# Kernel tuning notes

Measured on AMD Instinct MI355X. Metric: run time of the kernel, lower is better.

Reference implementation:

```python
import jax, jax.numpy as jnp
import numpy as np


def setup_inputs() -> dict:
    key = jax.random.key(0)
    ks = jax.random.split(key, 8)
    B, S, T, H, A = 4, 1024, 256, 512, 256
    return {
        "encoder_outputs": jax.random.normal(ks[0], (B, S, H), dtype=jnp.float32),
        "decoder_hidden": jax.random.normal(ks[1], (B, T, H), dtype=jnp.float32),
        "Wh": jax.random.normal(ks[2], (H, A), dtype=jnp.float32) * (1.0 / np.sqrt(H)),
        "bh": jax.random.normal(ks[3], (A,), dtype=jnp.float32) * 0.01,
        "Ws": jax.random.normal(ks[4], (H, A), dtype=jnp.float32) * (1.0 / np.sqrt(H)),
        "bs": jax.random.normal(ks[5], (A,), dtype=jnp.float32) * 0.01,
        "Wv": jax.random.normal(ks[6], (A, 1), dtype=jnp.float32) * (1.0 / np.sqrt(A)),
        "bv": jax.random.normal(ks[7], (1,), dtype=jnp.float32) * 0.01,
    }


def reference(encoder_outputs, decoder_hidden, Wh, bh, Ws, bs, Wv, bv):
    # encoder_outputs: [B, S, H], decoder_hidden: [B, T, H]
    eh = encoder_outputs @ Wh + bh          # [B, S, A]
    dh = decoder_hidden @ Ws + bs           # [B, T, A]
    # broadcast-add (torch's unsqueeze+repeat is just a broadcast), tanh, then v-projection
    energy = jnp.tanh(eh[:, None, :, :] + dh[:, :, None, :])  # [B, T, S, A]
    scores = jnp.einsum("btsa,a->bts", energy, Wv[:, 0]) + bv[0]  # [B, T, S]
    return jax.nn.softmax(scores, axis=2)
```

## Files before the change

### kernel.cpp

```cpp
#include <hip/hip_runtime.h>

#define B_ 4
#define S_ 1024
#define T_ 256
#define H_ 512
#define A_ 256

typedef __attribute__((ext_vector_type(8))) short short8;
typedef __attribute__((ext_vector_type(4))) float f32x4;

__device__ __forceinline__ float ex2(float x)   { return __builtin_amdgcn_exp2f(x); }
__device__ __forceinline__ float rcpf_(float x) { return __builtin_amdgcn_rcpf(x); }

#define K2F 2.8853900817779268f

__device__ __forceinline__ void split_bf16(float x, unsigned short& h, unsigned short& l)
{
    unsigned u = __float_as_uint(x);
    unsigned r = (u + 0x7FFFu + ((u >> 16) & 1u)) >> 16;
    h = (unsigned short)r;
    float hf = __uint_as_float(r << 16);
    float lo = x - hf;
    unsigned u2 = __float_as_uint(lo);
    l = (unsigned short)((u2 + 0x7FFFu + ((u2 >> 16) & 1u)) >> 16);
}

__global__ __launch_bounds__(256)
void prep_w(const float* __restrict__ Wh, const float* __restrict__ Wsm,
            unsigned short* __restrict__ WhTh, unsigned short* __restrict__ WhTl,
            unsigned short* __restrict__ WsTh, unsigned short* __restrict__ WsTl)
{
    __shared__ float lds[32][36];
    const int tid = threadIdx.x, bid = blockIdx.x;
    const int mat = bid >> 7, rem = bid & 127;
    const int k0 = (rem & 15) * 32, a0 = (rem >> 4) * 32;
    const float* W = mat ? Wsm : Wh;
    unsigned short* Oh = mat ? WsTh : WhTh;
    unsigned short* Ol = mat ? WsTl : WhTl;

    {
        int kl = tid >> 3, a4 = (tid & 7) * 4;
        float4 v = *(const float4*)&W[(size_t)(k0 + kl) * A_ + a0 + a4];
        lds[kl][a4] = v.x; lds[kl][a4 + 1] = v.y; lds[kl][a4 + 2] = v.z; lds[kl][a4 + 3] = v.w;
    }
    __syncthreads();
    {
        int al = tid >> 3, k4 = (tid & 7) * 4;
        unsigned short h[4], l[4];
        #pragma unroll
        for (int i = 0; i < 4; ++i) split_bf16(lds[k4 + i][al], h[i], l[i]);
        size_t o = (size_t)(a0 + al) * H_ + k0 + k4;
        *(ushort4*)&Oh[o] = make_ushort4(h[0], h[1], h[2], h[3]);
        *(ushort4*)&Ol[o] = make_ushort4(l[0], l[1], l[2], l[3]);
    }
}

__global__ __launch_bounds__(256)
void gemm_mfma(const float* __restrict__ enc, const float* __restrict__ dec,
               const unsigned short* __restrict__ WhTh, const unsigned short* __restrict__ WhTl,
               const unsigned short* __restrict__ WsTh, const unsigned short* __restrict__ WsTl,
               const float* __restrict__ bh, const float* __restrict__ bs,
               float* __restrict__ Ebuf, float* __restrict__ Dbuf)
{
    __shared__ short smem[8192];
    short* Ah = smem;
    short* Al = smem + 2048;
    short* Bh = smem + 4096;
    short* Bl = smem + 6144;

    const int tid = threadIdx.x, bid = blockIdx.x;
    const bool isE = bid < 256;
    int mb, nb;
    const float* Ag; const unsigned short* WTh; const unsigned short* WTl; const float* bias;
    if (isE) { mb = (bid & 63) * 64; nb = (bid >> 6) * 64; Ag = enc; WTh = WhTh; WTl = WhTl; bias = bh; }
    else { int b2 = bid - 256; mb = (b2 & 15) * 64; nb = (b2 >> 4) * 64; Ag = dec; WTh = WsTh; WTl = WsTl; bias = bs; }

    const int m_l = tid >> 2, q = tid & 3;
    const size_t arow = (size_t)(mb + m_l) * H_ + 8 * q;
    const size_t brow = (size_t)(nb + m_l) * H_ + 8 * q;
    const int woff = ((m_l >> 4) * 64 + (m_l & 15) + 16 * q) * 8;

    const int wave = tid >> 6, lane = tid & 63;
    const int wm = wave >> 1, wn = wave & 1;
    const int roffA = (2 * wm) * 512 + lane * 8;
    const int roffB = (2 * wn) * 512 + lane * 8;

    const int cl = lane & 15, rg = lane >> 4;
    const float bias0 = bias[nb + wn * 32 + cl];
    const float bias1 = bias[nb + wn * 32 + 16 + cl];

    f32x4 acc[2][2] = {};

    float4 aA = *(const float4*)&Ag[arow];
    float4 aB = *(const float4*)&Ag[arow + 4];
    short8 bHv = *(const short8*)&WTh[brow];
    short8 bLv = *(const short8*)&WTl[brow];

    for (int it = 0; it < 16; ++it) {
        __syncthreads();
        {
            float xs[8] = {aA.x, aA.y, aA.z, aA.w, aB.x, aB.y, aB.z, aB.w};
            short8 hv, lv;
            #pragma unroll
            for (int j = 0; j < 8; ++j) {
                unsigned short h, l; split_bf16(xs[j], h, l);
                hv[j] = (short)h; lv[j] = (short)l;
            }
            *(short8*)&Ah[woff] = hv;
            *(short8*)&Al[woff] = lv;
            *(short8*)&Bh[woff] = bHv;
            *(short8*)&Bl[woff] = bLv;
        }
        if (it < 15) {
            int kn = (it + 1) * 32;
            aA  = *(const float4*)&Ag[arow + kn];
            aB  = *(const float4*)&Ag[arow + kn + 4];
            bHv = *(const short8*)&WTh[brow + kn];
            bLv = *(const short8*)&WTl[brow + kn];
        }
        __syncthreads();
        short8 fAh0 = *(short8*)&Ah[roffA], fAh1 = *(short8*)&Ah[roffA + 512];
        short8 fAl0 = *(short8*)&Al[roffA], fAl1 = *(short8*)&Al[roffA + 512];
        short8 fBh0 = *(short8*)&Bh[roffB], fBh1 = *(short8*)&Bh[roffB + 512];
        short8 fBl0 = *(short8*)&Bl[roffB], fBl1 = *(short8*)&Bl[roffB + 512];
        acc[0][0] = __builtin_amdgcn_mfma_f32_16x16x32_bf16(fAh0, fBh0, acc[0][0], 0, 0, 0);
        acc[0][0] = __builtin_amdgcn_mfma_f32_16x16x32_bf16(fAh0, fBl0, acc[0][0], 0, 0, 0);
        acc[0][0] = __builtin_amdgcn_mfma_f32_16x16x32_bf16(fAl0, fBh0, acc[0][0], 0, 0, 0);
        acc[0][1] = __builtin_amdgcn_mfma_f32_16x16x32_bf16(fAh0, fBh1, acc[0][1], 0, 0, 0);
        acc[0][1] = __builtin_amdgcn_mfma_f32_16x16x32_bf16(fAh0, fBl1, acc[0][1], 0, 0, 0);
        acc[0][1] = __builtin_amdgcn_mfma_f32_16x16x32_bf16(fAl0, fBh1, acc[0][1], 0, 0, 0);
        acc[1][0] = __builtin_amdgcn_mfma_f32_16x16x32_bf16(fAh1, fBh0, acc[1][0], 0, 0, 0);
        acc[1][0] = __builtin_amdgcn_mfma_f32_16x16x32_bf16(fAh1, fBl0, acc[1][0], 0, 0, 0);
        acc[1][0] = __builtin_amdgcn_mfma_f32_16x16x32_bf16(fAl1, fBh0, acc[1][0], 0, 0, 0);
        acc[1][1] = __builtin_amdgcn_mfma_f32_16x16x32_bf16(fAh1, fBh1, acc[1][1], 0, 0, 0);
        acc[1][1] = __builtin_amdgcn_mfma_f32_16x16x32_bf16(fAh1, fBl1, acc[1][1], 0, 0, 0);
        acc[1][1] = __builtin_amdgcn_mfma_f32_16x16x32_bf16(fAl1, fBh1, acc[1][1], 0, 0, 0);
    }

    #pragma unroll
    for (int mf = 0; mf < 2; ++mf) {
        const int mg = mb + wm * 32 + mf * 16 + rg * 4;
        #pragma unroll
        for (int nf = 0; nf < 2; ++nf) {
            const int a = nb + wn * 32 + nf * 16 + cl;
            const float bb = nf ? bias1 : bias0;
            f32x4 ac = acc[mf][nf];
            float4 st;
            st.x = ex2((ac[0] + bb) * K2F);
            st.y = ex2((ac[1] + bb) * K2F);
            st.z = ex2((ac[2] + bb) * K2F);
            st.w = ex2((ac[3] + bb) * K2F);
            if (isE) {
                const int b = mg >> 10, s = mg & 1023;
                *(float4*)&Ebuf[(((size_t)b * A_ + a) << 10) + s] = st;
            } else {
                Dbuf[(size_t)(mg + 0) * A_ + a] = st.x;
                Dbuf[(size_t)(mg + 1) * A_ + a] = st.y;
                Dbuf[(size_t)(mg + 2) * A_ + a] = st.z;
                Dbuf[(size_t)(mg + 3) * A_ + a] = st.w;
            }
        }
    }
}

template<int AS>
__global__ __launch_bounds__(512)
void score_partial(const float* __restrict__ E, const float* __restrict__ D,
                   const float* __restrict__ Wv,
                   float* __restrict__ P0, float* __restrict__ P1,
                   float* __restrict__ P2, float* __restrict__ P3)
{
    constexpr int ABLK = 256 / AS;
    constexpr int NG   = ABLK / 4;

    const int tid = threadIdx.x;
    const int bid = blockIdx.x;
    const int b   = bid / (64 * AS);
    const int rem = bid % (64 * AS);
    const int h   = rem & (AS - 1);
    const int t0  = (rem / AS) * 4;
    const int abase = h * ABLK;

    __shared__ float Dsh[4][ABLK];
    __shared__ float Wsh[ABLK];

    if (tid < ABLK) {
        int r = tid / (ABLK / 4), c4 = (tid % (ABLK / 4)) << 2;
        *(float4*)&Dsh[r][c4] = *(const float4*)&D[((size_t)b * T_ + t0 + r) * A_ + abase + c4];
    } else if (tid < ABLK + ABLK / 4) {
        int c4 = (tid - ABLK) << 2;
        *(float4*)&Wsh[c4] = *(const float4*)&Wv[abase + c4];
    }
    __syncthreads();

    const int s0 = tid << 1;
    const float* Eb = E + ((size_t)b * A_ + abase) * S_ + s0;

    float accx[4] = {}, accy[4] = {};
    float2 evA[4], evB[4];

    #pragma unroll
    for (int j = 0; j < 4; ++j) evA[j] = *(const float2*)&Eb[(size_t)j * S_];

    auto compute = [&](const float2* ev, int g) {
        float4 w = *(const float4*)&Wsh[g * 4];
        #pragma unroll
        for (int t = 0; t < 4; ++t) {
            float4 d = *(const float4*)&Dsh[t][g * 4];
            {
                float q0 = fmaf(ev[0].x, d.x, 1.0f);
                float q1 = fmaf(ev[1].x, d.y, 1.0f);
                float q2 = fmaf(ev[2].x, d.z, 1.0f);
                float q3 = fmaf(ev[3].x, d.w, 1.0f);
                float q01 = q0 * q1, q23 = q2 * q3;
                float n1 = fmaf(w.x, q1, w.y * q0);
                float n2 = fmaf(w.z, q3, w.w * q2);
                float num = fmaf(n1, q23, n2 * q01);
                accx[t] = fmaf(num, rcpf_(q01 * q23), accx[t]);
            }
            {
                float q0 = fmaf(ev[0].y, d.x, 1.0f);
                float q1 = fmaf(ev[1].y, d.y, 1.0f);
                float q2 = fmaf(ev[2].y, d.z, 1.0f);
                float q3 = fmaf(ev[3].y, d.w, 1.0f);
                float q01 = q0 * q1, q23 = q2 * q3;
                float n1 = fmaf(w.x, q1, w.y * q0);
                float n2 = fmaf(w.z, q3, w.w * q2);
                float num = fmaf(n1, q23, n2 * q01);
                accy[t] = fmaf(num, rcpf_(q01 * q23), accy[t]);
            }
        }
    };

    for (int g = 0; g < NG; g += 2) {
        #pragma unroll
        for (int j = 0; j < 4; ++j) evB[j] = *(const float2*)&Eb[(size_t)((g + 1) * 4 + j) * S_];
        compute(evA, g);
        if (g + 2 < NG) {
            #pragma unroll
            for (int j = 0; j < 4; ++j) evA[j] = *(const float2*)&Eb[(size_t)((g + 2) * 4 + j) * S_];
        }
        compute(evB, g + 1);
    }

    float* Pd = (h == 0) ? P0 : (h == 1) ? P1 : (h == 2) ? P2 : P3;
    #pragma unroll
    for (int t = 0; t < 4; ++t) {
        float2 o; o.x = accx[t]; o.y = accy[t];
        *(float2*)&Pd[((size_t)b * T_ + t0 + t) * S_ + s0] = o;
    }
}

template<int NP>
__global__ __launch_bounds__(256)
void merge_softmax(const float* __restrict__ P1, const float* __restrict__ P2,
                   const float* __restrict__ P3, float* __restrict__ outp)
{
    const int row = blockIdx.x;
    const int tid = threadIdx.x;
    const int lane = tid & 63, wid = tid >> 6;
    __shared__ float red[4];

    float* o = outp + (size_t)row * S_;
    const int s4 = tid << 2;

    float4 a = *(const float4*)&o[s4];
    {
        float4 c = *(const float4*)&P1[(size_t)row * S_ + s4];
        a.x += c.x; a.y += c.y; a.z += c.z; a.w += c.w;
    }
    if (NP >= 4) {
        float4 c = *(const float4*)&P2[(size_t)row * S_ + s4];
        a.x += c.x; a.y += c.y; a.z += c.z; a.w += c.w;
        float4 e = *(const float4*)&P3[(size_t)row * S_ + s4];
        a.x += e.x; a.y += e.y; a.z += e.z; a.w += e.w;
    }
    float e0 = ex2(a.x * -K2F);
    float e1 = ex2(a.y * -K2F);
    float e2 = ex2(a.z * -K2F);
    float e3 = ex2(a.w * -K2F);

    float ssum = (e0 + e1) + (e2 + e3);
    #pragma unroll
    for (int off = 32; off > 0; off >>= 1) ssum += __shfl_xor(ssum, off, 64);
    if (lane == 0) red[wid] = ssum;
    __syncthreads();
    float tot = (red[0] + red[1]) + (red[2] + red[3]);
    float inv = 1.0f / tot;

    *(float4*)&o[s4] = make_float4(e0 * inv, e1 * inv, e2 * inv, e3 * inv);
}

extern "C" void kernel_launch(void* const* d_in, const int* in_sizes, int n_in,
                              void* d_out, int out_size, void* d_ws, size_t ws_size,
                              hipStream_t stream)
{
    const float* enc = (const float*)d_in[0];
    const float* dec = (const float*)d_in[1];
    const float* Wh  = (const float*)d_in[2];
    const float* bh  = (const float*)d_in[3];
    const float* Wsm = (const float*)d_in[4];
    const float* bs  = (const float*)d_in[5];
    const float* Wv  = (const float*)d_in[6];

    char* ws = (char*)d_ws;
    float* Ebuf = (float*)ws;
    float* Dbuf = (float*)(ws + (4 << 20));
    unsigned short* wt = (unsigned short*)(ws + (5 << 20));
    unsigned short* WhTh = wt;
    unsigned short* WhTl = wt + 131072;
    unsigned short* WsTh = wt + 262144;
    unsigned short* WsTl = wt + 393216;
    float* P1 = (float*)(ws + (6 << 20));
    float* P2 = (float*)(ws + (10 << 20));
    float* P3 = (float*)(ws + (14 << 20));
    float* P0 = (float*)d_out;

    prep_w<<<256, 256, 0, stream>>>(Wh, Wsm, WhTh, WhTl, WsTh, WsTl);
    gemm_mfma<<<320, 256, 0, stream>>>(enc, dec, WhTh, WhTl, WsTh, WsTl,
                                       bh, bs, Ebuf, Dbuf);
    if (ws_size >= (size_t)(18 << 20)) {
        score_partial<4><<<B_ * 256, 512, 0, stream>>>(Ebuf, Dbuf, Wv, P0, P1, P2, P3);
        merge_softmax<4><<<B_ * T_, 256, 0, stream>>>(P1, P2, P3, (float*)d_out);
    } else {
        score_partial<2><<<B_ * 128, 512, 0, stream>>>(Ebuf, Dbuf, Wv, P0, P1, P2, P3);
        merge_softmax<2><<<B_ * T_, 256, 0, stream>>>(P1, P2, P3, (float*)d_out);
    }
}
```

Measured before the change: 56.09 us.

## Split A dimension 16 ways in score kernel and halve GEMM N-tile

The GEMM now uses 32-wide N tiles, doubling its grid to 640 blocks, and only half the threads load B. A new score_partial16 kernel splits the A dimension into 16 slices of 16 channels each, using 4096 blocks, with each thread handling two s positions. It writes 16 partial score planes to workspace, which merge_softmax16 sums before the softmax. This raises parallelism and occupancy but needs a 64MB partial buffer, adds extra global traffic for the merge, and only runs when the workspace is at least 72MB.

```diff
diff --git a/kernel.cpp b/kernel.cpp
--- a/kernel.cpp
+++ b/kernel.cpp
@@ -62,39 +62,43 @@
                const float* __restrict__ bh, const float* __restrict__ bs,
                float* __restrict__ Ebuf, float* __restrict__ Dbuf)
 {
-    __shared__ short smem[8192];
+    __shared__ short smem[6144];
     short* Ah = smem;
     short* Al = smem + 2048;
     short* Bh = smem + 4096;
-    short* Bl = smem + 6144;
+    short* Bl = smem + 5120;
 
     const int tid = threadIdx.x, bid = blockIdx.x;
-    const bool isE = bid < 256;
+    const bool isE = bid < 512;
     int mb, nb;
     const float* Ag; const unsigned short* WTh; const unsigned short* WTl; const float* bias;
-    if (isE) { mb = (bid & 63) * 64; nb = (bid >> 6) * 64; Ag = enc; WTh = WhTh; WTl = WhTl; bias = bh; }
-    else { int b2 = bid - 256; mb = (b2 & 15) * 64; nb = (b2 >> 4) * 64; Ag = dec; WTh = WsTh; WTl = WsTl; bias = bs; }
+    if (isE) { mb = (bid & 63) * 64; nb = (bid >> 6) * 32; Ag = enc; WTh = WhTh; WTl = WhTl; bias = bh; }
+    else { int b2 = bid - 512; mb = (b2 & 15) * 64; nb = (b2 >> 4) * 32; Ag = dec; WTh = WsTh; WTl = WsTl; bias = bs; }
 
     const int m_l = tid >> 2, q = tid & 3;
     const size_t arow = (size_t)(mb + m_l) * H_ + 8 * q;
-    const size_t brow = (size_t)(nb + m_l) * H_ + 8 * q;
-    const int woff = ((m_l >> 4) * 64 + (m_l & 15) + 16 * q) * 8;
+    const int woffA = ((m_l >> 4) * 64 + (m_l & 15) + 16 * q) * 8;
+    const bool doB = tid < 128;
+    const size_t brow = (size_t)(nb + (m_l & 31)) * H_ + 8 * q;
+    const int woffB = (((m_l & 31) >> 4) * 64 + (m_l & 15) + 16 * q) * 8;
 
     const int wave = tid >> 6, lane = tid & 63;
     const int wm = wave >> 1, wn = wave & 1;
     const int roffA = (2 * wm) * 512 + lane * 8;
-    const int roffB = (2 * wn) * 512 + lane * 8;
+    const int roffB = wn * 512 + lane * 8;
 
     const int cl = lane & 15, rg = lane >> 4;
-    const float bias0 = bias[nb + wn * 32 + cl];
-    const float bias1 = bias[nb + wn * 32 + 16 + cl];
-
-    f32x4 acc[2][2] = {};
+    const float bias0 = bias[nb + wn * 16 + cl];
+
+    f32x4 acc[2] = {};
 
     float4 aA = *(const float4*)&Ag[arow];
     float4 aB = *(const float4*)&Ag[arow + 4];
-    short8 bHv = *(const short8*)&WTh[brow];
-    short8 bLv = *(const short8*)&WTl[brow];
+    short8 bHv, bLv;
+    if (doB) {
+        bHv = *(const short8*)&WTh[brow];
+        bLv = *(const short8*)&WTl[brow];
+    }
 
     for (int it = 0; it < 16; ++it) {
         __syncthreads();
@@ -106,61 +110,152 @@
                 unsigned short h, l; split_bf16(xs[j], h, l);
                 hv[j] = (short)h; lv[j] = (short)l;
             }
-            *(short8*)&Ah[woff] = hv;
-            *(short8*)&Al[woff] = lv;
-            *(short8*)&Bh[woff] = bHv;
-            *(short8*)&Bl[woff] = bLv;
+            *(short8*)&Ah[woffA] = hv;
+            *(short8*)&Al[woffA] = lv;
+            if (doB) {
+                *(short8*)&Bh[woffB] = bHv;
+                *(short8*)&Bl[woffB] = bLv;
+            }
         }
         if (it < 15) {
             int kn = (it + 1) * 32;
             aA  = *(const float4*)&Ag[arow + kn];
             aB  = *(const float4*)&Ag[arow + kn + 4];
-            bHv = *(const short8*)&WTh[brow + kn];
-            bLv = *(const short8*)&WTl[brow + kn];
+            if (doB) {
+                bHv = *(const short8*)&WTh[brow + kn];
+                bLv = *(const short8*)&WTl[brow + kn];
+            }
         }
         __syncthreads();
-        short8 fAh0 = *(short8*)&Ah[roffA], fAh1 = *(short8*)&Ah[roffA + 512];
-        short8 fAl0 = *(short8*)&Al[roffA], fAl1 = *(short8*)&Al[roffA + 512];
-        short8 fBh0 = *(short8*)&Bh[roffB], fBh1 = *(short8*)&Bh[roffB + 512];
-        short8 fBl0 = *(short8*)&Bl[roffB], fBl1 = *(short8*)&Bl[roffB + 512];
-        acc[0][0] = __builtin_amdgcn_mfma_f32_16x16x32_bf16(fAh0, fBh0, acc[0][0], 0, 0, 0);
-        acc[0][0] = __builtin_amdgcn_mfma_f32_16x16x32_bf16(fAh0, fBl0, acc[0][0], 0, 0, 0);
-        acc[0][0] = __builtin_amdgcn_mfma_f32_16x16x32_bf16(fAl0, fBh0, acc[0][0], 0, 0, 0);
-        acc[0][1] = __builtin_amdgcn_mfma_f32_16x16x32_bf16(fAh0, fBh1, acc[0][1], 0, 0, 0);
-        acc[0][1] = __builtin_amdgcn_mfma_f32_16x16x32_bf16(fAh0, fBl1, acc[0][1], 0, 0, 0);
-        acc[0][1] = __builtin_amdgcn_mfma_f32_16x16x32_bf16(fAl0, fBh1, acc[0][1], 0, 0, 0);
-        acc[1][0] = __builtin_amdgcn_mfma_f32_16x16x32_bf16(fAh1, fBh0, acc[1][0], 0, 0, 0);
-        acc[1][0] = __builtin_amdgcn_mfma_f32_16x16x32_bf16(fAh1, fBl0, acc[1][0], 0, 0, 0);
-        acc[1][0] = __builtin_amdgcn_mfma_f32_16x16x32_bf16(fAl1, fBh0, acc[1][0], 0, 0, 0);
-        acc[1][1] = __builtin_amdgcn_mfma_f32_16x16x32_bf16(fAh1, fBh1, acc[1][1], 0, 0, 0);
-        acc[1][1] = __builtin_amdgcn_mfma_f32_16x16x32_bf16(fAh1, fBl1, acc[1][1], 0, 0, 0);
-        acc[1][1] = __builtin_amdgcn_mfma_f32_16x16x32_bf16(fAl1, fBh1, acc[1][1], 0, 0, 0);
+        short8 fBh = *(short8*)&Bh[roffB];
+        short8 fBl = *(short8*)&Bl[roffB];
+        #pragma unroll
+        for (int mf = 0; mf < 2; ++mf) {
+            short8 fAh = *(short8*)&Ah[roffA + mf * 512];
+            short8 fAl = *(short8*)&Al[roffA + mf * 512];
+            acc[mf] = __builtin_amdgcn_mfma_f32_16x16x32_bf16(fAh, fBh, acc[mf], 0, 0, 0);
+            acc[mf] = __builtin_amdgcn_mfma_f32_16x16x32_bf16(fAh, fBl, acc[mf], 0, 0, 0);
+            acc[mf] = __builtin_amdgcn_mfma_f32_16x16x32_bf16(fAl, fBh, acc[mf], 0, 0, 0);
+        }
     }
 
     #pragma unroll
     for (int mf = 0; mf < 2; ++mf) {
         const int mg = mb + wm * 32 + mf * 16 + rg * 4;
+        const int a = nb + wn * 16 + cl;
+        f32x4 ac = acc[mf];
+        float4 st;
+        st.x = ex2((ac[0] + bias0) * K2F);
+        st.y = ex2((ac[1] + bias0) * K2F);
+        st.z = ex2((ac[2] + bias0) * K2F);
+        st.w = ex2((ac[3] + bias0) * K2F);
+        if (isE) {
+            const int b = mg >> 10, s = mg & 1023;
+            *(float4*)&Ebuf[(((size_t)b * A_ + a) << 10) + s] = st;
+        } else {
+            Dbuf[(size_t)(mg + 0) * A_ + a] = st.x;
+            Dbuf[(size_t)(mg + 1) * A_ + a] = st.y;
+            Dbuf[(size_t)(mg + 2) * A_ + a] = st.z;
+            Dbuf[(size_t)(mg + 3) * A_ + a] = st.w;
+        }
+    }
+}
+
+#define GROUP4(e0, e1, e2, e3, A0)                                           \
+    _Pragma("unroll")                                                        \
+    for (int t = 0; t < 4; ++t) {                                            \
+        { float q0 = fmaf(e0.x, ds[t][(A0)],     1.0f);                      \
+          float q1 = fmaf(e1.x, ds[t][(A0) + 1], 1.0f);                      \
+          float q2 = fmaf(e2.x, ds[t][(A0) + 2], 1.0f);                      \
+          float q3 = fmaf(e3.x, ds[t][(A0) + 3], 1.0f);                      \
+          float q01 = q0 * q1, q23 = q2 * q3;                                \
+          float n1 = fmaf(wv[(A0)], q1, wv[(A0) + 1] * q0);                  \
+          float n2 = fmaf(wv[(A0) + 2], q3, wv[(A0) + 3] * q2);              \
+          float num = fmaf(n1, q23, n2 * q01);                               \
+          accx[t] = fmaf(num, rcpf_(q01 * q23), accx[t]); }                  \
+        { float q0 = fmaf(e0.y, ds[t][(A0)],     1.0f);                      \
+          float q1 = fmaf(e1.y, ds[t][(A0) + 1], 1.0f);                      \
+          float q2 = fmaf(e2.y, ds[t][(A0) + 2], 1.0f);                      \
+          float q3 = fmaf(e3.y, ds[t][(A0) + 3], 1.0f);                      \
+          float q01 = q0 * q1, q23 = q2 * q3;                                \
+          float n1 = fmaf(wv[(A0)], q1, wv[(A0) + 1] * q0);                  \
+          float n2 = fmaf(wv[(A0) + 2], q3, wv[(A0) + 3] * q2);              \
+          float num = fmaf(n1, q23, n2 * q01);                               \
+          accy[t] = fmaf(num, rcpf_(q01 * q23), accy[t]); }                  \
+    }
+
+__global__ __launch_bounds__(512)
+void score_partial16(const float* __restrict__ E, const float* __restrict__ D,
+                     const float* __restrict__ Wv, float* __restrict__ P)
+{
+    const int tid = threadIdx.x;
+    const int bid = blockIdx.x;
+    const int b   = bid >> 10;
+    const int rem = bid & 1023;
+    const int h   = rem & 15;
+    const int t0  = (rem >> 4) * 4;
+    const int abase = h * 16;
+
+    float ds[4][16], wv[16];
+    #pragma unroll
+    for (int t = 0; t < 4; ++t)
         #pragma unroll
-        for (int nf = 0; nf < 2; ++nf) {
-            const int a = nb + wn * 32 + nf * 16 + cl;
-            const float bb = nf ? bias1 : bias0;
-            f32x4 ac = acc[mf][nf];
-            float4 st;
-            st.x = ex2((ac[0] + bb) * K2F);
-            st.y = ex2((ac[1] + bb) * K2F);
-            st.z = ex2((ac[2] + bb) * K2F);
-            st.w = ex2((ac[3] + bb) * K2F);
-            if (isE) {
-                const int b = mg >> 10, s = mg & 1023;
-                *(float4*)&Ebuf[(((size_t)b * A_ + a) << 10) + s] = st;
-            } else {
-                Dbuf[(size_t)(mg + 0) * A_ + a] = st.x;
-                Dbuf[(size_t)(mg + 1) * A_ + a] = st.y;
-                Dbuf[(size_t)(mg + 2) * A_ + a] = st.z;
-                Dbuf[(size_t)(mg + 3) * A_ + a] = st.w;
-            }
-        }
-    }
+        for (int i = 0; i < 16; ++i)
+            ds[t][i] = D[((size_t)b * T_ + t0 + t) * A_ + abase + i];
+    #pragma unroll
+    for (int i = 0; i < 16; ++i) wv[i] = Wv[abase + i];
+
+    const int s0 = tid << 1;
+    const float* Eb = E + ((size_t)b * A_ + abase) * S_ + s0;
+
+    float accx[4] = {}, accy[4] = {};
+    float2 ev[8];
+
+    #pragma unroll
+    for (int j = 0; j < 8; ++j) ev[j] = *(const float2*)&Eb[(size_t)j * S_];
+    GROUP4(ev[0], ev[1], ev[2], ev[3], 0);
+    GROUP4(ev[4], ev[5], ev[6], ev[7], 4);
+    #pragma unroll
+    for (int j = 0; j < 8; ++j) ev[j] = *(const float2*)&Eb[(size_t)(8 + j) * S_];
+    GROUP4(ev[0], ev[1], ev[2], ev[3], 8);
+    GROUP4(ev[4], ev[5], ev[6], ev[7], 12);
+
+    #pragma unroll
+    for (int t = 0; t < 4; ++t) {
+        float2 o; o.x = accx[t]; o.y = accy[t];
+        *(float2*)&P[((size_t)h * (B_ * T_) + (size_t)b * T_ + t0 + t) * S_ + s0] = o;
+    }
+}
+
+__global__ __launch_bounds__(256)
+void merge_softmax16(const float* __restrict__ P, float* __restrict__ outp)
+{
+    const int row = blockIdx.x;
+    const int tid = threadIdx.x;
+    const int lane = tid & 63, wid = tid >> 6;
+    __shared__ float red[4];
+
+    const int s4 = tid << 2;
+    float4 a = *(const float4*)&P[(size_t)row * S_ + s4];
+    #pragma unroll
+    for (int hh = 1; hh < 16; ++hh) {
+        float4 c = *(const float4*)&P[((size_t)hh * (B_ * T_) + row) * S_ + s4];
+        a.x += c.x; a.y += c.y; a.z += c.z; a.w += c.w;
+    }
+    float e0 = ex2(a.x * -K2F);
+    float e1 = ex2(a.y * -K2F);
+    float e2 = ex2(a.z * -K2F);
+    float e3 = ex2(a.w * -K2F);
+
+    float ssum = (e0 + e1) + (e2 + e3);
+    #pragma unroll
+    for (int off = 32; off > 0; off >>= 1) ssum += __shfl_xor(ssum, off, 64);
+    if (lane == 0) red[wid] = ssum;
+    __syncthreads();
+    float tot = (red[0] + red[1]) + (red[2] + red[3]);
+    float inv = 1.0f / tot;
+
+    *(float4*)&outp[(size_t)row * S_ + s4] = make_float4(e0 * inv, e1 * inv, e2 * inv, e3 * inv);
 }
 
 template<int AS>
@@ -311,19 +406,26 @@
     unsigned short* WhTl = wt + 131072;
     unsigned short* WsTh = wt + 262144;
     unsigned short* WsTl = wt + 393216;
-    float* P1 = (float*)(ws + (6 << 20));
-    float* P2 = (float*)(ws + (10 << 20));
-    float* P3 = (float*)(ws + (14 << 20));
-    float* P0 = (float*)d_out;
 
     prep_w<<<256, 256, 0, stream>>>(Wh, Wsm, WhTh, WhTl, WsTh, WsTl);
-    gemm_mfma<<<320, 256, 0, stream>>>(enc, dec, WhTh, WhTl, WsTh, WsTl,
+    gemm_mfma<<<640, 256, 0, stream>>>(enc, dec, WhTh, WhTl, WsTh, WsTl,
                                        bh, bs, Ebuf, Dbuf);
-    if (ws_size >= (size_t)(18 << 20)) {
+
+    if (ws_size >= (size_t)(72 << 20)) {
+        float* P16 = (float*)(ws + (6 << 20));
+        score_partial16<<<4096, 512, 0, stream>>>(Ebuf, Dbuf, Wv, P16);
+        merge_softmax16<<<B_ * T_, 256, 0, stream>>>(P16, (float*)d_out);
+    } else if (ws_size >= (size_t)(18 << 20)) {
+        float* P1 = (float*)(ws + (6 << 20));
+        float* P2 = (float*)(ws + (10 << 20));
+        float* P3 = (float*)(ws + (14 << 20));
+        float* P0 = (float*)d_out;
         score_partial<4><<<B_ * 256, 512, 0, stream>>>(Ebuf, Dbuf, Wv, P0, P1, P2, P3);
         merge_softmax<4><<<B_ * T_, 256, 0, stream>>>(P1, P2, P3, (float*)d_out);
     } else {
-        score_partial<2><<<B_ * 128, 512, 0, stream>>>(Ebuf, Dbuf, Wv, P0, P1, P2, P3);
-        merge_softmax<2><<<B_ * T_, 256, 0, stream>>>(P1, P2, P3, (float*)d_out);
-    }
-}
+        float* P1 = (float*)(ws + (6 << 20));
+        float* P0 = (float*)d_out;
+        score_partial<2><<<B_ * 128, 512, 0, stream>>>(Ebuf, Dbuf, Wv, P0, P1, nullptr, nullptr);
+        merge_softmax<2><<<B_ * T_, 256, 0, stream>>>(P1, nullptr, nullptr, (float*)d_out);
+    }
+}
```

Result: slower. 65.33 us (+16.5%).

## Broadcast D and Wv via readlane and widen per-thread s tile in score kernel

Applied to the files above, without the earlier changes.

Replaces the LDS-staged D and Wv operands in the score kernel with per-lane register loads broadcast through readlane, so inner-loop operands become scalars. Each thread now covers four s positions with 256-thread blocks, and tanh terms are combined in pairs rather than quads per reciprocal. This removes LDS traffic and the barrier but doubles reciprocal count per term. The workspace-size fallback path is dropped.

```diff
diff --git a/kernel.cpp b/kernel.cpp
--- a/kernel.cpp
+++ b/kernel.cpp
@@ -13,6 +13,8 @@
 __device__ __forceinline__ float rcpf_(float x) { return __builtin_amdgcn_rcpf(x); }
 
 #define K2F 2.8853900817779268f
+
+#define RL(v, l) __uint_as_float(__builtin_amdgcn_readlane(__float_as_uint(v), (l)))
 
 __device__ __forceinline__ void split_bf16(float x, unsigned short& h, unsigned short& l)
 {
@@ -163,98 +165,78 @@
     }
 }
 
-template<int AS>
-__global__ __launch_bounds__(512)
-void score_partial(const float* __restrict__ E, const float* __restrict__ D,
-                   const float* __restrict__ Wv,
-                   float* __restrict__ P0, float* __restrict__ P1,
-                   float* __restrict__ P2, float* __restrict__ P3)
-{
-    constexpr int ABLK = 256 / AS;
-    constexpr int NG   = ABLK / 4;
-
+__global__ __launch_bounds__(256)
+void score_rl(const float* __restrict__ E, const float* __restrict__ D,
+              const float* __restrict__ Wv,
+              float* __restrict__ P0, float* __restrict__ P1,
+              float* __restrict__ P2, float* __restrict__ P3)
+{
     const int tid = threadIdx.x;
     const int bid = blockIdx.x;
-    const int b   = bid / (64 * AS);
-    const int rem = bid % (64 * AS);
-    const int h   = rem & (AS - 1);
-    const int t0  = (rem / AS) * 4;
-    const int abase = h * ABLK;
-
-    __shared__ float Dsh[4][ABLK];
-    __shared__ float Wsh[ABLK];
-
-    if (tid < ABLK) {
-        int r = tid / (ABLK / 4), c4 = (tid % (ABLK / 4)) << 2;
-        *(float4*)&Dsh[r][c4] = *(const float4*)&D[((size_t)b * T_ + t0 + r) * A_ + abase + c4];
-    } else if (tid < ABLK + ABLK / 4) {
-        int c4 = (tid - ABLK) << 2;
-        *(float4*)&Wsh[c4] = *(const float4*)&Wv[abase + c4];
-    }
-    __syncthreads();
-
-    const int s0 = tid << 1;
+    const int b   = bid >> 8;
+    const int rem = bid & 255;
+    const int h   = rem & 3;
+    const int t0  = (rem >> 2) * 4;
+    const int abase = h * 64;
+    const int lane = tid & 63;
+
+    const float vd0 = D[((size_t)b * T_ + t0 + 0) * A_ + abase + lane];
+    const float vd1 = D[((size_t)b * T_ + t0 + 1) * A_ + abase + lane];
+    const float vd2 = D[((size_t)b * T_ + t0 + 2) * A_ + abase + lane];
+    const float vd3 = D[((size_t)b * T_ + t0 + 3) * A_ + abase + lane];
+    const float vw  = Wv[abase + lane];
+
+    const int s0 = tid << 2;
     const float* Eb = E + ((size_t)b * A_ + abase) * S_ + s0;
 
-    float accx[4] = {}, accy[4] = {};
-    float2 evA[4], evB[4];
-
-    #pragma unroll
-    for (int j = 0; j < 4; ++j) evA[j] = *(const float2*)&Eb[(size_t)j * S_];
-
-    auto compute = [&](const float2* ev, int g) {
-        float4 w = *(const float4*)&Wsh[g * 4];
-        #pragma unroll
-        for (int t = 0; t < 4; ++t) {
-            float4 d = *(const float4*)&Dsh[t][g * 4];
-            {
-                float q0 = fmaf(ev[0].x, d.x, 1.0f);
-                float q1 = fmaf(ev[1].x, d.y, 1.0f);
-                float q2 = fmaf(ev[2].x, d.z, 1.0f);
-                float q3 = fmaf(ev[3].x, d.w, 1.0f);
-                float q01 = q0 * q1, q23 = q2 * q3;
-                float n1 = fmaf(w.x, q1, w.y * q0);
-                float n2 = fmaf(w.z, q3, w.w * q2);
-                float num = fmaf(n1, q23, n2 * q01);
-                accx[t] = fmaf(num, rcpf_(q01 * q23), accx[t]);
-            }
-            {
-                float q0 = fmaf(ev[0].y, d.x, 1.0f);
-                float q1 = fmaf(ev[1].y, d.y, 1.0f);
-                float q2 = fmaf(ev[2].y, d.z, 1.0f);
-                float q3 = fmaf(ev[3].y, d.w, 1.0f);
-                float q01 = q0 * q1, q23 = q2 * q3;
-                float n1 = fmaf(w.x, q1, w.y * q0);
-                float n2 = fmaf(w.z, q3, w.w * q2);
-                float num = fmaf(n1, q23, n2 * q01);
-                accy[t] = fmaf(num, rcpf_(q01 * q23), accy[t]);
-            }
+    float acc[4][4] = {};
+
+    float4 eA0 = *(const float4*)&Eb[0];
+    float4 eA1 = *(const float4*)&Eb[S_];
+    float4 eB0, eB1;
+
+#define PAIR_RL(E0, E1, L0, L1)                                              \
+    {                                                                        \
+        float w0 = RL(vw, (L0)), w1 = RL(vw, (L1));                          \
+        float d0_[4] = {RL(vd0,(L0)), RL(vd1,(L0)), RL(vd2,(L0)), RL(vd3,(L0))}; \
+        float d1_[4] = {RL(vd0,(L1)), RL(vd1,(L1)), RL(vd2,(L1)), RL(vd3,(L1))}; \
+        const float* e0 = (const float*)&(E0);                               \
+        const float* e1 = (const float*)&(E1);                               \
+        _Pragma("unroll")                                                    \
+        for (int t = 0; t < 4; ++t) {                                        \
+            _Pragma("unroll")                                                \
+            for (int k = 0; k < 4; ++k) {                                    \
+                float q0 = fmaf(e0[k], d0_[t], 1.0f);                        \
+                float q1 = fmaf(e1[k], d1_[t], 1.0f);                        \
+                float num = fmaf(w0, q1, w1 * q0);                           \
+                acc[t][k] = fmaf(num, rcpf_(q0 * q1), acc[t][k]);            \
+            }                                                                \
+        }                                                                    \
+    }
+
+    for (int g = 0; g < 32; g += 2) {
+        eB0 = *(const float4*)&Eb[(size_t)(2 * g + 2) * S_];
+        eB1 = *(const float4*)&Eb[(size_t)(2 * g + 3) * S_];
+        PAIR_RL(eA0, eA1, 2 * g, 2 * g + 1);
+        if (g + 2 < 32) {
+            eA0 = *(const float4*)&Eb[(size_t)(2 * g + 4) * S_];
+            eA1 = *(const float4*)&Eb[(size_t)(2 * g + 5) * S_];
         }
-    };
-
-    for (int g = 0; g < NG; g += 2) {
-        #pragma unroll
-        for (int j = 0; j < 4; ++j) evB[j] = *(const float2*)&Eb[(size_t)((g + 1) * 4 + j) * S_];
-        compute(evA, g);
-        if (g + 2 < NG) {
-            #pragma unroll
-            for (int j = 0; j < 4; ++j) evA[j] = *(const float2*)&Eb[(size_t)((g + 2) * 4 + j) * S_];
-        }
-        compute(evB, g + 1);
-    }
+        PAIR_RL(eB0, eB1, 2 * g + 2, 2 * g + 3);
+    }
+#undef PAIR_RL
 
     float* Pd = (h == 0) ? P0 : (h == 1) ? P1 : (h == 2) ? P2 : P3;
     #pragma unroll
     for (int t = 0; t < 4; ++t) {
-        float2 o; o.x = accx[t]; o.y = accy[t];
-        *(float2*)&Pd[((size_t)b * T_ + t0 + t) * S_ + s0] = o;
-    }
-}
-
-template<int NP>
+        float4 o = make_float4(acc[t][0], acc[t][1], acc[t][2], acc[t][3]);
+        *(float4*)&Pd[((size_t)b * T_ + t0 + t) * S_ + s0] = o;
+    }
+}
+
 __global__ __launch_bounds__(256)
-void merge_softmax(const float* __restrict__ P1, const float* __restrict__ P2,
-                   const float* __restrict__ P3, float* __restrict__ outp)
+void merge_softmax4(const float* __restrict__ P1, const float* __restrict__ P2,
+                    const float* __restrict__ P3, float* __restrict__ outp)
 {
     const int row = blockIdx.x;
     const int tid = threadIdx.x;
@@ -269,7 +251,7 @@
         float4 c = *(const float4*)&P1[(size_t)row * S_ + s4];
         a.x += c.x; a.y += c.y; a.z += c.z; a.w += c.w;
     }
-    if (NP >= 4) {
+    {
         float4 c = *(const float4*)&P2[(size_t)row * S_ + s4];
         a.x += c.x; a.y += c.y; a.z += c.z; a.w += c.w;
         float4 e = *(const float4*)&P3[(size_t)row * S_ + s4];
@@ -311,19 +293,15 @@
     unsigned short* WhTl = wt + 131072;
     unsigned short* WsTh = wt + 262144;
     unsigned short* WsTl = wt + 393216;
+
+    prep_w<<<256, 256, 0, stream>>>(Wh, Wsm, WhTh, WhTl, WsTh, WsTl);
+    gemm_mfma<<<320, 256, 0, stream>>>(enc, dec, WhTh, WhTl, WsTh, WsTl,
+                                       bh, bs, Ebuf, Dbuf);
+
+    float* P0 = (float*)d_out;
     float* P1 = (float*)(ws + (6 << 20));
     float* P2 = (float*)(ws + (10 << 20));
     float* P3 = (float*)(ws + (14 << 20));
-    float* P0 = (float*)d_out;
-
-    prep_w<<<256, 256, 0, stream>>>(Wh, Wsm, WhTh, WhTl, WsTh, WsTl);
-    gemm_mfma<<<320, 256, 0, stream>>>(enc, dec, WhTh, WhTl, WsTh, WsTl,
-                                       bh, bs, Ebuf, Dbuf);
-    if (ws_size >= (size_t)(18 << 20)) {
-        score_partial<4><<<B_ * 256, 512, 0, stream>>>(Ebuf, Dbuf, Wv, P0, P1, P2, P3);
-        merge_softmax<4><<<B_ * T_, 256, 0, stream>>>(P1, P2, P3, (float*)d_out);
-    } else {
-        score_partial<2><<<B_ * 128, 512, 0, stream>>>(Ebuf, Dbuf, Wv, P0, P1, P2, P3);
-        merge_softmax<2><<<B_ * T_, 256, 0, stream>>>(P1, P2, P3, (float*)d_out);
-    }
-}
+    score_rl<<<B_ * 256, 256, 0, stream>>>(Ebuf, Dbuf, Wv, P0, P1, P2, P3);
+    merge_softmax4<<<B_ * T_, 256, 0, stream>>>(P1, P2, P3, (float*)d_out);
+}
```

New measurement: 59.88 us. +6.8%, slower.
